# Optimization experiments

Hardware: AMD Instinct MI355X
Metric: run time of the kernel (lower is better)

## Reference

```python
import math
import jax, jax.numpy as jnp
from jax import lax
import numpy as np

B = 2048
C = 32000
TAU = math.log(32000.0)
LAM = 1.0
BATCH_SIZE = 2048.0
TEMP = 4.0


def lambertw(y, iters=8):
    """Principal-branch Lambert W for real y >= -1/e via Halley iterations."""
    # branch-point expansion init for small y, asymptotic log init for large y
    ey1 = jnp.maximum(jnp.e * y + 1.0, 0.0)
    w_small = -1.0 + jnp.sqrt(2.0 * ey1)
    ys = jnp.maximum(y, 1.0 + 1e-6)
    w_big = jnp.log(ys) - jnp.log(jnp.maximum(jnp.log(ys), 1e-6))
    w = jnp.where(y < 1.0, w_small, w_big)
    for _ in range(iters):
        ew = jnp.exp(w)
        f = w * ew - y
        wp1 = w + 1.0
        denom = ew * wp1 - (w + 2.0) * f / (2.0 * jnp.where(jnp.abs(wp1) > 1e-6, wp1, 1e-6))
        denom = jnp.where(jnp.abs(denom) > 1e-12, denom, 1e-12)
        w = w - f / denom
    return w


def _per_sample_loss(logits, teacher_outputs, targets, ones):
    # cross entropy per sample
    logp = jax.nn.log_softmax(logits, axis=-1)  # [B, C]
    ce = -jnp.take_along_axis(logp, targets[:, None], axis=1)[:, 0]  # [B]
    # temperature-scaled KL(teacher || student), summed over classes
    logp_T = jax.nn.log_softmax(logits / TEMP, axis=-1)
    p_t = jax.nn.softmax(teacher_outputs / TEMP, axis=-1)
    kl = jnp.sum(p_t * (jnp.log(p_t) - logp_T), axis=-1)  # [B]
    return ones[:, 0] * ce + TEMP * TEMP * ones[:, 1] * kl  # [B]


def reference(logits, teacher_outputs, targets, ones):
    base = _per_sample_loss(logits, teacher_outputs, targets, ones)  # [B]
    # sigma computed from detached loss (torch .detach() + cpu numpy round-trip)
    l_i = lax.stop_gradient(base)
    y = 0.5 * jnp.maximum(-2.0 / jnp.e, (l_i - TAU) / LAM)
    sigma = jnp.exp(-lambertw(y))  # [B], no gradient flows through
    loss = (base - TAU) * sigma + LAM * jnp.log(sigma) ** 2
    return loss.sum() / BATCH_SIZE


def setup_inputs() -> dict:
    key = jax.random.key(0)
    k1, k2, k3 = jax.random.split(key, 3)
    return {
        "logits": jax.random.normal(k1, (B, C), dtype=jnp.float32),
        "teacher_outputs": jax.random.normal(k2, (B, C), dtype=jnp.float32),
        "targets": jax.random.randint(k3, (B,), 0, C, dtype=jnp.int32),
        "ones": jnp.ones((B, 2), dtype=jnp.float32),
    }
```

## Files before the change

### kernel.cpp

```cpp
#include <hip/hip_runtime.h>
#include <math.h>

#define NCLASS 32000
#define NROWS  2048
#define TEMP_F 4.0f

#define TAU_D 10.373491181781864
#define E_D   2.718281828459045

__device__ __forceinline__ double lambertw_d(double y) {
    double ey1 = fmax(E_D * y + 1.0, 0.0);
    double w_small = -1.0 + sqrt(2.0 * ey1);
    double ys = fmax(y, 1.0 + 1e-6);
    double ly = log(ys);
    double w_big = ly - log(fmax(ly, 1e-6));
    double w = (y < 1.0) ? w_small : w_big;
#pragma unroll
    for (int i = 0; i < 8; ++i) {
        double ew = exp(w);
        double f = w * ew - y;
        double wp1 = w + 1.0;
        double safe_wp1 = (fabs(wp1) > 1e-6) ? wp1 : 1e-6;
        double denom = ew * wp1 - (w + 2.0) * f / (2.0 * safe_wp1);
        if (!(fabs(denom) > 1e-12)) denom = 1e-12;
        w = w - f / denom;
    }
    return w;
}

__device__ __forceinline__ void upd(float x, float t,
                                    float& s1, float& sT, float& st,
                                    float& A, float& Bv) {
    s1 += __expf(x);
    sT += __expf(x * 0.25f);
    float e = __expf(t * 0.25f);
    st += e;
    A  = fmaf(e, t, A);
    Bv = fmaf(e, x, Bv);
}

__global__ __launch_bounds__(256) void superloss_kernel(
    const float* __restrict__ logits,
    const float* __restrict__ teacher,
    const int*   __restrict__ targets,
    const float* __restrict__ ones,
    float* __restrict__ out)
{
    const int row = blockIdx.x;
    const size_t base_off = (size_t)row * NCLASS;
    const float4* lg = (const float4*)(logits  + base_off);
    const float4* tc = (const float4*)(teacher + base_off);

    float s1 = 0.f, sT = 0.f, st = 0.f, A = 0.f, Bv = 0.f;

    for (int j = threadIdx.x; j < NCLASS / 4; j += blockDim.x) {
        float4 xv = lg[j];
        float4 tv = tc[j];
        upd(xv.x, tv.x, s1, sT, st, A, Bv);
        upd(xv.y, tv.y, s1, sT, st, A, Bv);
        upd(xv.z, tv.z, s1, sT, st, A, Bv);
        upd(xv.w, tv.w, s1, sT, st, A, Bv);
    }

#pragma unroll
    for (int off = 32; off > 0; off >>= 1) {
        s1 += __shfl_down(s1, off);
        sT += __shfl_down(sT, off);
        st += __shfl_down(st, off);
        A  += __shfl_down(A,  off);
        Bv += __shfl_down(Bv, off);
    }

    __shared__ float red[4][5];
    const int wave = threadIdx.x >> 6;
    const int lane = threadIdx.x & 63;
    if (lane == 0) {
        red[wave][0] = s1; red[wave][1] = sT; red[wave][2] = st;
        red[wave][3] = A;  red[wave][4] = Bv;
    }
    __syncthreads();

    if (threadIdx.x == 0) {
        float fs1 = 0.f, fsT = 0.f, fst = 0.f, fA = 0.f, fB = 0.f;
#pragma unroll
        for (int w = 0; w < 4; ++w) {
            fs1 += red[w][0]; fsT += red[w][1]; fst += red[w][2];
            fA  += red[w][3]; fB  += red[w][4];
        }

        const float xt = logits[base_off + (size_t)targets[row]];
        const float o0 = ones[row * 2 + 0];
        const float o1 = ones[row * 2 + 1];

        double lse   = log((double)fs1);
        double lseT  = log((double)fsT);
        double lseTt = log((double)fst);

        double ce = lse - (double)xt;
        double kl = ((double)fA - (double)fB) / ((double)fst * (double)TEMP_F)
                    - lseTt + lseT;

        double base = (double)o0 * ce
                    + (double)(TEMP_F * TEMP_F) * (double)o1 * kl;

        double y = 0.5 * fmax(-2.0 / E_D, (base - TAU_D));
        double w = lambertw_d(y);
        double sigma = exp(-w);
        double loss = (base - TAU_D) * sigma + w * w;

        atomicAdd(out, (float)(loss / 2048.0));
    }
}

extern "C" void kernel_launch(void* const* d_in, const int* in_sizes, int n_in,
                              void* d_out, int out_size, void* d_ws, size_t ws_size,
                              hipStream_t stream) {
    const float* logits  = (const float*)d_in[0];
    const float* teacher = (const float*)d_in[1];
    const int*   targets = (const int*)d_in[2];
    const float* ones    = (const float*)d_in[3];
    float* out = (float*)d_out;

    hipMemsetAsync(out, 0, sizeof(float) * (size_t)out_size, stream);

    superloss_kernel<<<NROWS, 256, 0, stream>>>(logits, teacher, targets, ones, out);
}
```

Measured before the change: 517.8 us.

## Split row sums and finalize, software-pipeline loads, reuse one exp

The main kernel now uses 320 threads with a fixed five-stage, double-buffered schedule. Each thread issues five float4 loads of both inputs ahead of the compute, which keeps more memory requests in flight. The per-row Lambert-W finalization moves to a second kernel that runs one thread per row, so it no longer serializes one thread per block, and its block-level partial sums replace per-row atomics. exp(x) is now derived as the fourth power of exp(x/4), saving one transcendental per element at a small accuracy risk; the workspace round trip and extra launch add overhead.

```diff
diff --git a/kernel.cpp b/kernel.cpp
--- a/kernel.cpp
+++ b/kernel.cpp
@@ -3,7 +3,9 @@
 
 #define NCLASS 32000
 #define NROWS  2048
-#define TEMP_F 4.0f
+#define T1     320
+#define U      5
+#define STAGES 5
 
 #define TAU_D 10.373491181781864
 #define E_D   2.718281828459045
@@ -31,36 +33,58 @@
 __device__ __forceinline__ void upd(float x, float t,
                                     float& s1, float& sT, float& st,
                                     float& A, float& Bv) {
-    s1 += __expf(x);
-    sT += __expf(x * 0.25f);
-    float e = __expf(t * 0.25f);
-    st += e;
-    A  = fmaf(e, t, A);
-    Bv = fmaf(e, x, Bv);
+    float ex4 = __expf(x * 0.25f);
+    float ex2 = ex4 * ex4;
+    s1 += ex2 * ex2;
+    sT += ex4;
+    float et = __expf(t * 0.25f);
+    st += et;
+    A  = fmaf(et, t, A);
+    Bv = fmaf(et, x, Bv);
 }
 
-__global__ __launch_bounds__(256) void superloss_kernel(
+__global__ __launch_bounds__(T1) void sums_kernel(
     const float* __restrict__ logits,
     const float* __restrict__ teacher,
-    const int*   __restrict__ targets,
-    const float* __restrict__ ones,
-    float* __restrict__ out)
+    float* __restrict__ ws)
 {
     const int row = blockIdx.x;
-    const size_t base_off = (size_t)row * NCLASS;
-    const float4* lg = (const float4*)(logits  + base_off);
-    const float4* tc = (const float4*)(teacher + base_off);
+    const size_t base = (size_t)row * NCLASS;
+    const float4* __restrict__ lg = (const float4*)(logits  + base);
+    const float4* __restrict__ tc = (const float4*)(teacher + base);
+    const int tid = threadIdx.x;
 
     float s1 = 0.f, sT = 0.f, st = 0.f, A = 0.f, Bv = 0.f;
+    float4 xa[U], ta[U], xb[U], tb[U];
 
-    for (int j = threadIdx.x; j < NCLASS / 4; j += blockDim.x) {
-        float4 xv = lg[j];
-        float4 tv = tc[j];
-        upd(xv.x, tv.x, s1, sT, st, A, Bv);
-        upd(xv.y, tv.y, s1, sT, st, A, Bv);
-        upd(xv.z, tv.z, s1, sT, st, A, Bv);
-        upd(xv.w, tv.w, s1, sT, st, A, Bv);
-    }
+    auto load_stage = [&](float4* xd, float4* td, int s) {
+#pragma unroll
+        for (int k = 0; k < U; ++k) {
+            const int j = tid + (s * U + k) * T1;
+            xd[k] = lg[j];
+            td[k] = tc[j];
+        }
+    };
+    auto compute_stage = [&](const float4* xd, const float4* td) {
+#pragma unroll
+        for (int k = 0; k < U; ++k) {
+            upd(xd[k].x, td[k].x, s1, sT, st, A, Bv);
+            upd(xd[k].y, td[k].y, s1, sT, st, A, Bv);
+            upd(xd[k].z, td[k].z, s1, sT, st, A, Bv);
+            upd(xd[k].w, td[k].w, s1, sT, st, A, Bv);
+        }
+    };
+
+    load_stage(xa, ta, 0);
+    load_stage(xb, tb, 1);
+    compute_stage(xa, ta);
+    load_stage(xa, ta, 2);
+    compute_stage(xb, tb);
+    load_stage(xb, tb, 3);
+    compute_stage(xa, ta);
+    load_stage(xa, ta, 4);
+    compute_stage(xb, tb);
+    compute_stage(xa, ta);
 
 #pragma unroll
     for (int off = 32; off > 0; off >>= 1) {
@@ -71,44 +95,70 @@
         Bv += __shfl_down(Bv, off);
     }
 
-    __shared__ float red[4][5];
-    const int wave = threadIdx.x >> 6;
-    const int lane = threadIdx.x & 63;
+    __shared__ float red[T1 / 64][5];
+    const int wave = tid >> 6;
+    const int lane = tid & 63;
     if (lane == 0) {
         red[wave][0] = s1; red[wave][1] = sT; red[wave][2] = st;
         red[wave][3] = A;  red[wave][4] = Bv;
     }
     __syncthreads();
 
+    if (tid < 5) {
+        float acc = 0.f;
+#pragma unroll
+        for (int w = 0; w < T1 / 64; ++w) acc += red[w][tid];
+        ws[row * 5 + tid] = acc;
+    }
+}
+
+__global__ __launch_bounds__(256) void finalize_kernel(
+    const float* __restrict__ logits,
+    const int*   __restrict__ targets,
+    const float* __restrict__ ones,
+    const float* __restrict__ ws,
+    float* __restrict__ out)
+{
+    const int r = blockIdx.x * 256 + threadIdx.x;
+
+    const float fs1 = ws[r * 5 + 0];
+    const float fsT = ws[r * 5 + 1];
+    const float fst = ws[r * 5 + 2];
+    const float fA  = ws[r * 5 + 3];
+    const float fB  = ws[r * 5 + 4];
+
+    const float xt = logits[(size_t)r * NCLASS + (size_t)targets[r]];
+    const float o0 = ones[2 * r + 0];
+    const float o1 = ones[2 * r + 1];
+
+    const double lse   = log((double)fs1);
+    const double lseT  = log((double)fsT);
+    const double lseTt = log((double)fst);
+
+    const double ce = lse - (double)xt;
+    const double kl = ((double)fA - (double)fB) / ((double)fst * 4.0)
+                      - lseTt + lseT;
+
+    const double base = (double)o0 * ce + 16.0 * (double)o1 * kl;
+
+    const double y = 0.5 * fmax(-2.0 / E_D, (base - TAU_D));
+    const double w = lambertw_d(y);
+    const double sigma = exp(-w);
+    double loss = (base - TAU_D) * sigma + w * w;
+
+#pragma unroll
+    for (int off = 32; off > 0; off >>= 1)
+        loss += __shfl_down(loss, off);
+
+    __shared__ double red2[4];
+    const int wave = threadIdx.x >> 6;
+    const int lane = threadIdx.x & 63;
+    if (lane == 0) red2[wave] = loss;
+    __syncthreads();
+
     if (threadIdx.x == 0) {
-        float fs1 = 0.f, fsT = 0.f, fst = 0.f, fA = 0.f, fB = 0.f;
-#pragma unroll
-        for (int w = 0; w < 4; ++w) {
-            fs1 += red[w][0]; fsT += red[w][1]; fst += red[w][2];
-            fA  += red[w][3]; fB  += red[w][4];
-        }
-
-        const float xt = logits[base_off + (size_t)targets[row]];
-        const float o0 = ones[row * 2 + 0];
-        const float o1 = ones[row * 2 + 1];
-
-        double lse   = log((double)fs1);
-        double lseT  = log((double)fsT);
-        double lseTt = log((double)fst);
-
-        double ce = lse - (double)xt;
-        double kl = ((double)fA - (double)fB) / ((double)fst * (double)TEMP_F)
-                    - lseTt + lseT;
-
-        double base = (double)o0 * ce
-                    + (double)(TEMP_F * TEMP_F) * (double)o1 * kl;
-
-        double y = 0.5 * fmax(-2.0 / E_D, (base - TAU_D));
-        double w = lambertw_d(y);
-        double sigma = exp(-w);
-        double loss = (base - TAU_D) * sigma + w * w;
-
-        atomicAdd(out, (float)(loss / 2048.0));
+        double acc = red2[0] + red2[1] + red2[2] + red2[3];
+        atomicAdd(out, (float)(acc / 2048.0));
     }
 }
 
@@ -120,8 +170,10 @@
     const int*   targets = (const int*)d_in[2];
     const float* ones    = (const float*)d_in[3];
     float* out = (float*)d_out;
+    float* ws  = (float*)d_ws;
 
     hipMemsetAsync(out, 0, sizeof(float) * (size_t)out_size, stream);
 
-    superloss_kernel<<<NROWS, 256, 0, stream>>>(logits, teacher, targets, ones, out);
+    sums_kernel<<<NROWS, T1, 0, stream>>>(logits, teacher, ws);
+    finalize_kernel<<<NROWS / 256, 256, 0, stream>>>(logits, targets, ones, ws, out);
 }
```

New measurement: 502.3 us. -3.0%, faster.
